# Performance work log

Hardware: AMD Instinct MI355X
Metric: run time of the kernel (lower is better)

Reference implementation:

```python
import jax, jax.numpy as jnp
import numpy as np

B, W, H, C = 4, 32, 32, 128   # image feature map
S, D = 256, 512               # text seq len, text embed dim
NC = 64                       # num_channels (attention inner dim)


def setup_inputs() -> dict:
    key = jax.random.key(0)
    ks = jax.random.split(key, 16)
    def dense(k, din, dout):
        return jax.random.normal(k, (din, dout), jnp.float32) / np.sqrt(din)
    return {
        "x": jax.random.normal(ks[0], (B, W, H, C), jnp.float32),
        "s": jax.random.normal(ks[1], (B, S, D), jnp.float32),
        "a": jax.random.randint(ks[2], (B, S), 0, 2).astype(jnp.float32),
        "Wq": dense(ks[3], C, NC),  "bq": jnp.zeros((NC,), jnp.float32),
        "Wkx": dense(ks[4], C, NC), "bkx": jnp.zeros((NC,), jnp.float32),
        "Wvx": dense(ks[5], C, NC), "bvx": jnp.zeros((NC,), jnp.float32),
        "Wks": dense(ks[6], D, NC), "bks": jnp.zeros((NC,), jnp.float32),
        "Wvs": dense(ks[7], D, NC), "bvs": jnp.zeros((NC,), jnp.float32),
        "Wout": dense(ks[8], NC, C), "bout": jnp.zeros((C,), jnp.float32),
        "ln_scale": jnp.ones((C,), jnp.float32),
        "ln_bias": jnp.zeros((C,), jnp.float32),
    }


def reference(x, s, a, Wq, bq, Wkx, bkx, Wvx, bvx, Wks, bks, Wvs, bvs,
              Wout, bout, ln_scale, ln_bias):
    nc = Wq.shape[-1]
    # mask text embeddings: repeat(a,'b s -> b s d') * s
    te = s * a[:, :, None]
    # projections
    q = x @ Wq + bq            # (b,w,h,c)
    kx = x @ Wkx + bkx         # (b,w,h,c)
    vx = x @ Vx_dummy if False else x @ Wvx + bvx
    ks = te @ Wks + bks        # (b,s,c)
    vs = te @ Wvs + bvs        # (b,s,c)
    # broadcast-add spatial and text keys/values -> (b,w,h,s,c)
    k = kx[:, :, :, None, :] + ks[:, None, None, :, :]
    v = vx[:, :, :, None, :] + vs[:, None, None, :, :]
    # attention matrix over channels: v^T @ k contracted over s -> (b,w,h,c,c)
    attn = jnp.einsum('bwhsc,bwhsd->bwhcd', v, k) / jnp.sqrt(jnp.asarray(nc, x.dtype))
    attn = jax.nn.softmax(attn, axis=-1)
    # q applied through the channel-channel attention -> (b,w,h,c)
    out = jnp.einsum('bwhj,bwhjk->bwhk', q, attn)
    # output projection back to x channels, residual, layernorm
    out = out @ Wout + bout
    x = x + out
    mu = jnp.mean(x, axis=-1, keepdims=True)
    var = jnp.var(x, axis=-1, keepdims=True)
    x = (x - mu) * jax.lax.rsqrt(var + 1e-6) * ln_scale + ln_bias
    return x
```

## Files before the change

kernel.cpp:

```cpp
#include <hip/hip_runtime.h>
#include <hip/hip_bf16.h>

#define BB 4
#define SS 256
#define DD 512
#define CC 128
#define NC 64
#define PXB 4

__global__ __launch_bounds__(256) void fused_proj_kernel(
    const float* __restrict__ x,
    const float* __restrict__ Wq,  const float* __restrict__ bq,
    const float* __restrict__ Wkx, const float* __restrict__ bkx,
    const float* __restrict__ Wvx, const float* __restrict__ bvx,
    const float* __restrict__ s, const float* __restrict__ a,
    const float* __restrict__ Wks, const float* __restrict__ bks,
    const float* __restrict__ Wvs, const float* __restrict__ bvs,
    float* __restrict__ P, float* __restrict__ ksw, float* __restrict__ vsw)
{
    __shared__ float tel[2][DD];
    __shared__ float part[2][2][2][NC];
    __shared__ float xl[8][CC];

    const int t = threadIdx.x;
    const int w = t >> 6, lane = t & 63;

    if (blockIdx.x < 512) {
        const int px0 = blockIdx.x * 8;
        {
            const float4* x4 = (const float4*)(x + (size_t)px0 * CC);
            ((float4*)&xl[0][0])[t] = x4[t];
        }
        __syncthreads();
        if (w < 3) {
            const float* __restrict__ Wm = (w == 0) ? Wq : (w == 1 ? Wkx : Wvx);
            const float* __restrict__ bm = (w == 0) ? bq : (w == 1 ? bkx : bvx);
            const int ksub = lane >> 4;
            const int cg = (lane & 15) * 4;
            float4 acc[8] = {};
            #pragma unroll 4
            for (int j = 0; j < 32; ++j) {
                const int k = 4 * j + ksub;
                const float4 wv = *(const float4*)(Wm + (size_t)k * NC + cg);
                #pragma unroll
                for (int px = 0; px < 8; ++px) {
                    const float xv = xl[px][k];
                    acc[px].x = fmaf(xv, wv.x, acc[px].x);
                    acc[px].y = fmaf(xv, wv.y, acc[px].y);
                    acc[px].z = fmaf(xv, wv.z, acc[px].z);
                    acc[px].w = fmaf(xv, wv.w, acc[px].w);
                }
            }
            #pragma unroll
            for (int px = 0; px < 8; ++px) {
                #pragma unroll
                for (int off = 16; off <= 32; off <<= 1) {
                    acc[px].x += __shfl_down(acc[px].x, off);
                    acc[px].y += __shfl_down(acc[px].y, off);
                    acc[px].z += __shfl_down(acc[px].z, off);
                    acc[px].w += __shfl_down(acc[px].w, off);
                }
            }
            if (ksub == 0) {
                const float4 bb = *(const float4*)(bm + cg);
                #pragma unroll
                for (int px = 0; px < 8; ++px) {
                    float4 v;
                    v.x = acc[px].x + bb.x; v.y = acc[px].y + bb.y;
                    v.z = acc[px].z + bb.z; v.w = acc[px].w + bb.w;
                    *(float4*)(P + (size_t)(px0 + px) * 192 + w * 64 + cg) = v;
                }
            }
        }
    } else {
        const int row0 = (blockIdx.x - 512) * 2;
        {
            const float4* s4 = (const float4*)(s + (size_t)row0 * DD);
            const int r = t >> 7;
            const float am = a[row0 + r];
            float4 v = s4[t];
            v.x *= am; v.y *= am; v.z *= am; v.w *= am;
            ((float4*)&tel[0][0])[t] = v;
        }
        __syncthreads();

        const int m = w & 1, h = w >> 1;
        const int kb = h * 256;
        const int cg = (lane & 15) * 4;
        const int ksub = lane >> 4;
        const float* __restrict__ Wm = m ? Wvs : Wks;

        float4 acc0 = {0,0,0,0}, acc1 = {0,0,0,0};
        #pragma unroll 4
        for (int j = 0; j < 64; ++j) {
            const int k = kb + 4 * j + ksub;
            const float4 wv = *(const float4*)(Wm + (size_t)k * NC + cg);
            const float t0 = tel[0][k];
            const float t1 = tel[1][k];
            acc0.x = fmaf(t0, wv.x, acc0.x); acc0.y = fmaf(t0, wv.y, acc0.y);
            acc0.z = fmaf(t0, wv.z, acc0.z); acc0.w = fmaf(t0, wv.w, acc0.w);
            acc1.x = fmaf(t1, wv.x, acc1.x); acc1.y = fmaf(t1, wv.y, acc1.y);
            acc1.z = fmaf(t1, wv.z, acc1.z); acc1.w = fmaf(t1, wv.w, acc1.w);
        }
        #pragma unroll
        for (int off = 16; off <= 32; off <<= 1) {
            acc0.x += __shfl_down(acc0.x, off); acc0.y += __shfl_down(acc0.y, off);
            acc0.z += __shfl_down(acc0.z, off); acc0.w += __shfl_down(acc0.w, off);
            acc1.x += __shfl_down(acc1.x, off); acc1.y += __shfl_down(acc1.y, off);
            acc1.z += __shfl_down(acc1.z, off); acc1.w += __shfl_down(acc1.w, off);
        }
        if (lane < 16) {
            *(float4*)&part[m][h][0][cg] = acc0;
            *(float4*)&part[m][h][1][cg] = acc1;
        }
        __syncthreads();

        {
            const int mm = t >> 7, r = (t >> 6) & 1, col = t & 63;
            const float v = part[mm][0][r][col] + part[mm][1][r][col]
                          + (mm ? bvs[col] : bks[col]);
            float* dst = mm ? vsw : ksw;
            dst[(size_t)(row0 + r) * NC + col] = v;
        }
    }
}

__global__ __launch_bounds__(256) void reduce_kernel(
    const float* __restrict__ ksw, const float* __restrict__ vsw,
    float* __restrict__ Mw, float* __restrict__ Ksw, float* __restrict__ Vsw)
{
    __shared__ float pm[4][NC], pk[4][NC], pv[4];
    const int t = threadIdx.x, w = t >> 6, d = t & 63;
    const int b = blockIdx.x >> 6, c = blockIdx.x & 63;
    const float* __restrict__ vsb = vsw + (size_t)b * SS * NC;
    const float* __restrict__ ksb = ksw + (size_t)b * SS * NC;
    float acc = 0.f, ks_ = 0.f, vs_ = 0.f;
    #pragma unroll 4
    for (int j = 0; j < 64; ++j) {
        const int s2 = w * 64 + j;
        const float vv = vsb[s2 * NC + c];
        const float kv = ksb[s2 * NC + d];
        acc = fmaf(vv, kv, acc);
        ks_ += kv; vs_ += vv;
    }
    pm[w][d] = acc; pk[w][d] = ks_;
    if (d == 0) pv[w] = vs_;
    __syncthreads();
    if (t < 64) {
        Mw[((size_t)b * NC + c) * NC + t] = pm[0][t] + pm[1][t] + pm[2][t] + pm[3][t];
        if (c == 0) Ksw[b * NC + t] = pk[0][t] + pk[1][t] + pk[2][t] + pk[3][t];
        if (t == 0) Vsw[b * NC + c] = pv[0] + pv[1] + pv[2] + pv[3];
    }
}

__global__ __launch_bounds__(256) void pixel_kernel(
    const float* __restrict__ x, const float* __restrict__ P,
    const float* __restrict__ Wout, const float* __restrict__ bout,
    const float* __restrict__ ln_scale, const float* __restrict__ ln_bias,
    const float* __restrict__ Mw, const float* __restrict__ Ksw,
    const float* __restrict__ Vsw,
    float* __restrict__ out)
{
    __shared__ float Ml[NC * 65];
    __shared__ float projl[PXB][192];
    __shared__ float xl[PXB][CC];
    __shared__ float rsl[PXB][NC];
    __shared__ float mxl[PXB][NC];
    __shared__ float outl[PXB][NC];
    __shared__ float Ksl[NC], Vsl[NC];
    __shared__ float redl[2][2][4];

    const int t = threadIdx.x;
    const int w = t >> 6, lane = t & 63;
    const int px0g = blockIdx.x * PXB;
    const int b = px0g >> 10;

    {
        const float4* P4 = (const float4*)(P + (size_t)px0g * 192);
        for (int i = t; i < PXB * 192 / 4; i += 256)
            ((float4*)&projl[0][0])[i] = P4[i];
        const float4* x4 = (const float4*)(x + (size_t)px0g * CC);
        for (int i = t; i < PXB * CC / 4; i += 256)
            ((float4*)&xl[0][0])[i] = x4[i];
        const float* Mb = Mw + (size_t)b * NC * NC;
        for (int i = t; i < NC * NC; i += 256)
            Ml[(i >> 6) * 65 + (i & 63)] = Mb[i];
        if (t < NC) { Ksl[t] = Ksw[b * NC + t]; Vsl[t] = Vsw[b * NC + t]; }
    }
    __syncthreads();

    {
        const int px = w, c = lane;
        const float vxc = projl[px][128 + c];
        const float qc  = projl[px][c];
        const float uc  = fmaf(256.0f, vxc, Vsl[c]);
        float mx = -3.4e38f;
        #pragma unroll
        for (int d = 0; d < NC; ++d) {
            const float A = fmaf(uc, projl[px][64 + d],
                                 fmaf(vxc, Ksl[d], Ml[c * 65 + d])) * 0.125f;
            mx = fmaxf(mx, A);
        }
        float sum = 0.f;
        #pragma unroll
        for (int d = 0; d < NC; ++d) {
            const float A = fmaf(uc, projl[px][64 + d],
                                 fmaf(vxc, Ksl[d], Ml[c * 65 + d])) * 0.125f;
            sum += __expf(A - mx);
        }
        rsl[px][c] = qc / sum;
        mxl[px][c] = mx;
    }
    __syncthreads();

    {
        const int px = w, d = lane;
        const float kxd = projl[px][64 + d];
        const float Ksd = Ksl[d];
        float acc = 0.f;
        #pragma unroll 4
        for (int c = 0; c < NC; ++c) {
            const float vxc = projl[px][128 + c];
            const float uc = fmaf(256.0f, vxc, Vsl[c]);
            const float A = fmaf(uc, kxd, fmaf(vxc, Ksd, Ml[c * 65 + d])) * 0.125f;
            acc = fmaf(rsl[px][c], __expf(A - mxl[px][c]), acc);
        }
        outl[px][d] = acc;
    }
    __syncthreads();

    {
        const int col = t & 127;
        const int pxg = t >> 7;
        const int px0 = 2 * pxg, px1 = px0 + 1;
        float acc0 = 0.f, acc1 = 0.f;
        #pragma unroll 4
        for (int k = 0; k < NC; ++k) {
            const float wv = Wout[k * CC + col];
            acc0 = fmaf(outl[px0][k], wv, acc0);
            acc1 = fmaf(outl[px1][k], wv, acc1);
        }
        const float bb = bout[col];
        const float y0 = acc0 + bb + xl[px0][col];
        const float y1 = acc1 + bb + xl[px1][col];

        float s10 = y0, s20 = y0 * y0, s11 = y1, s21 = y1 * y1;
        #pragma unroll
        for (int off = 32; off >= 1; off >>= 1) {
            s10 += __shfl_down(s10, off);
            s20 += __shfl_down(s20, off);
            s11 += __shfl_down(s11, off);
            s21 += __shfl_down(s21, off);
        }
        const int half = (t >> 6) & 1;
        if (lane == 0) {
            redl[pxg][half][0] = s10; redl[pxg][half][1] = s20;
            redl[pxg][half][2] = s11; redl[pxg][half][3] = s21;
        }
        __syncthreads();
        const float S10 = redl[pxg][0][0] + redl[pxg][1][0];
        const float S20 = redl[pxg][0][1] + redl[pxg][1][1];
        const float S11 = redl[pxg][0][2] + redl[pxg][1][2];
        const float S21 = redl[pxg][0][3] + redl[pxg][1][3];
        const float mu0 = S10 * (1.f / 128.f);
        const float var0 = S20 * (1.f / 128.f) - mu0 * mu0;
        const float mu1 = S11 * (1.f / 128.f);
        const float var1 = S21 * (1.f / 128.f) - mu1 * mu1;
        const float r0 = rsqrtf(var0 + 1e-6f), r1 = rsqrtf(var1 + 1e-6f);
        const float gg = ln_scale[col], be = ln_bias[col];
        out[(size_t)(px0g + px0) * CC + col] = (y0 - mu0) * r0 * gg + be;
        out[(size_t)(px0g + px1) * CC + col] = (y1 - mu1) * r1 * gg + be;
    }
}

extern "C" void kernel_launch(void* const* d_in, const int* in_sizes, int n_in,
                              void* d_out, int out_size, void* d_ws, size_t ws_size,
                              hipStream_t stream) {
    const float* x        = (const float*)d_in[0];
    const float* s        = (const float*)d_in[1];
    const float* a        = (const float*)d_in[2];
    const float* Wq       = (const float*)d_in[3];
    const float* bq       = (const float*)d_in[4];
    const float* Wkx      = (const float*)d_in[5];
    const float* bkx      = (const float*)d_in[6];
    const float* Wvx      = (const float*)d_in[7];
    const float* bvx      = (const float*)d_in[8];
    const float* Wks      = (const float*)d_in[9];
    const float* bks      = (const float*)d_in[10];
    const float* Wvs      = (const float*)d_in[11];
    const float* bvs      = (const float*)d_in[12];
    const float* Wout     = (const float*)d_in[13];
    const float* bout     = (const float*)d_in[14];
    const float* ln_scale = (const float*)d_in[15];
    const float* ln_bias  = (const float*)d_in[16];

    float* ws  = (float*)d_ws;
    float* ksw = ws;
    float* vsw = ws + 65536;
    float* Mw  = ws + 131072;
    float* Ksw = ws + 147456;
    float* Vsw = ws + 147712;
    float* Pw  = ws + 147968;

    fused_proj_kernel<<<1024, 256, 0, stream>>>(
        x, Wq, bq, Wkx, bkx, Wvx, bvx, s, a, Wks, bks, Wvs, bvs, Pw, ksw, vsw);
    reduce_kernel<<<BB * NC, 256, 0, stream>>>(ksw, vsw, Mw, Ksw, Vsw);
    pixel_kernel<<<(BB * 1024) / PXB, 256, 0, stream>>>(
        x, Pw, Wout, bout, ln_scale, ln_bias, Mw, Ksw, Vsw, (float*)d_out);
}
```

Before: 118.2 us.

## Fuse text-key/value reduction into projection kernel via atomics

Removes the separate reduce kernel. Each text block now projects 8 rows instead of 2 and computes its partial contributions to the channel-channel matrix M and to the key and value sums directly, accumulating them into global memory with atomicAdd after a memset. This saves a kernel launch and the workspace round trip for ks and vs. In exchange it adds 4096 atomics per text block across 128 blocks and a memset call, and the float summation order becomes nondeterministic.

```diff
diff --git a/kernel.cpp b/kernel.cpp
--- a/kernel.cpp
+++ b/kernel.cpp
@@ -7,44 +7,136 @@
 #define CC 128
 #define NC 64
 #define PXB 4
-
-__global__ __launch_bounds__(256) void fused_proj_kernel(
+#define NTEXT 128
+
+struct XRole { float xl[8][CC]; };
+struct TRole { float tel[8][DD];
+               float part[2][2][8][NC];
+               float ksl[8][NC]; float vsl[8][NC]; };
+union ProjSH { XRole xr; TRole tr; };
+
+__global__ __launch_bounds__(256) void proj_kernel(
     const float* __restrict__ x,
     const float* __restrict__ Wq,  const float* __restrict__ bq,
     const float* __restrict__ Wkx, const float* __restrict__ bkx,
     const float* __restrict__ Wvx, const float* __restrict__ bvx,
-    const float* __restrict__ s, const float* __restrict__ a,
+    const float* __restrict__ s,   const float* __restrict__ a,
     const float* __restrict__ Wks, const float* __restrict__ bks,
     const float* __restrict__ Wvs, const float* __restrict__ bvs,
-    float* __restrict__ P, float* __restrict__ ksw, float* __restrict__ vsw)
+    float* __restrict__ P, float* __restrict__ Mw,
+    float* __restrict__ Ksw, float* __restrict__ Vsw)
 {
-    __shared__ float tel[2][DD];
-    __shared__ float part[2][2][2][NC];
-    __shared__ float xl[8][CC];
-
+    __shared__ ProjSH sh;
     const int t = threadIdx.x;
     const int w = t >> 6, lane = t & 63;
-
-    if (blockIdx.x < 512) {
-        const int px0 = blockIdx.x * 8;
+    const int blk = blockIdx.x;
+
+    if (blk < NTEXT) {
+        const int row0 = blk * 8;
+        const int b = row0 >> 8;
         {
-            const float4* x4 = (const float4*)(x + (size_t)px0 * CC);
-            ((float4*)&xl[0][0])[t] = x4[t];
-        }
+            const float4* s4 = (const float4*)(s + (size_t)row0 * DD);
+            #pragma unroll
+            for (int j = 0; j < 4; ++j) {
+                const int i = t + j * 256;
+                const int r = i >> 7;
+                const float am = a[row0 + r];
+                float4 v = s4[i];
+                v.x *= am; v.y *= am; v.z *= am; v.w *= am;
+                ((float4*)&sh.tr.tel[0][0])[i] = v;
+            }
+        }
+        __syncthreads();
+
+        const int m = w & 1, h = w >> 1;
+        const int kb = h * 256;
+        const int cg4 = (lane & 15) * 4;
+        const int ksub = lane >> 4;
+        const float* __restrict__ Wm = m ? Wvs : Wks;
+
+        float4 acc[8] = {};
+        #pragma unroll 2
+        for (int j = 0; j < 64; ++j) {
+            const int k = kb + 4 * j + ksub;
+            const float4 wv = *(const float4*)(Wm + (size_t)k * NC + cg4);
+            #pragma unroll
+            for (int r = 0; r < 8; ++r) {
+                const float tv = sh.tr.tel[r][k];
+                acc[r].x = fmaf(tv, wv.x, acc[r].x);
+                acc[r].y = fmaf(tv, wv.y, acc[r].y);
+                acc[r].z = fmaf(tv, wv.z, acc[r].z);
+                acc[r].w = fmaf(tv, wv.w, acc[r].w);
+            }
+        }
+        #pragma unroll
+        for (int r = 0; r < 8; ++r) {
+            #pragma unroll
+            for (int off = 16; off <= 32; off <<= 1) {
+                acc[r].x += __shfl_down(acc[r].x, off);
+                acc[r].y += __shfl_down(acc[r].y, off);
+                acc[r].z += __shfl_down(acc[r].z, off);
+                acc[r].w += __shfl_down(acc[r].w, off);
+            }
+        }
+        if (lane < 16) {
+            #pragma unroll
+            for (int r = 0; r < 8; ++r)
+                *(float4*)&sh.tr.part[m][h][r][cg4] = acc[r];
+        }
+        __syncthreads();
+
+        #pragma unroll
+        for (int i = t; i < 1024; i += 256) {
+            const int mm = i >> 9;
+            const int r = (i >> 6) & 7;
+            const int col = i & 63;
+            const float v = sh.tr.part[mm][0][r][col] + sh.tr.part[mm][1][r][col]
+                          + (mm ? bvs[col] : bks[col]);
+            if (mm) sh.tr.vsl[r][col] = v; else sh.tr.ksl[r][col] = v;
+        }
+        __syncthreads();
+
+        if (w == 0) {
+            float sk = 0.f;
+            #pragma unroll
+            for (int r = 0; r < 8; ++r) sk += sh.tr.ksl[r][lane];
+            atomicAdd(&Ksw[b * NC + lane], sk);
+        } else if (w == 1) {
+            float sv = 0.f;
+            #pragma unroll
+            for (int r = 0; r < 8; ++r) sv += sh.tr.vsl[r][lane];
+            atomicAdd(&Vsw[b * NC + lane], sv);
+        }
+
+        float* __restrict__ Mb = Mw + (size_t)b * NC * NC;
+        #pragma unroll 4
+        for (int j = 0; j < 16; ++j) {
+            const int idx = t + j * 256;
+            const int c = idx >> 6;
+            float pm = 0.f;
+            #pragma unroll
+            for (int r = 0; r < 8; ++r)
+                pm = fmaf(sh.tr.vsl[r][c], sh.tr.ksl[r][lane], pm);
+            atomicAdd(Mb + idx, pm);
+        }
+    } else {
+        const int px0 = (blk - NTEXT) * 8;
+        ((float4*)&sh.xr.xl[0][0])[t] =
+            ((const float4*)(x + (size_t)px0 * CC))[t];
         __syncthreads();
         if (w < 3) {
             const float* __restrict__ Wm = (w == 0) ? Wq : (w == 1 ? Wkx : Wvx);
             const float* __restrict__ bm = (w == 0) ? bq : (w == 1 ? bkx : bvx);
             const int ksub = lane >> 4;
-            const int cg = (lane & 15) * 4;
+            const int cg4 = (lane & 15) * 4;
             float4 acc[8] = {};
             #pragma unroll 4
             for (int j = 0; j < 32; ++j) {
                 const int k = 4 * j + ksub;
-                const float4 wv = *(const float4*)(Wm + (size_t)k * NC + cg);
+                const float4 wv = *(const float4*)(Wm + (size_t)k * NC + cg4);
                 #pragma unroll
                 for (int px = 0; px < 8; ++px) {
-                    const float xv = xl[px][k];
+                    const float xv = sh.xr.xl[px][k];
                     acc[px].x = fmaf(xv, wv.x, acc[px].x);
                     acc[px].y = fmaf(xv, wv.y, acc[px].y);
                     acc[px].z = fmaf(xv, wv.z, acc[px].z);
@@ -62,94 +154,16 @@
                 }
             }
             if (ksub == 0) {
-                const float4 bb = *(const float4*)(bm + cg);
+                const float4 bb = *(const float4*)(bm + cg4);
                 #pragma unroll
                 for (int px = 0; px < 8; ++px) {
                     float4 v;
                     v.x = acc[px].x + bb.x; v.y = acc[px].y + bb.y;
                     v.z = acc[px].z + bb.z; v.w = acc[px].w + bb.w;
-                    *(float4*)(P + (size_t)(px0 + px) * 192 + w * 64 + cg) = v;
+                    *(float4*)(P + (size_t)(px0 + px) * 192 + w * 64 + cg4) = v;
                 }
             }
         }
-    } else {
-        const int row0 = (blockIdx.x - 512) * 2;
-        {
-            const float4* s4 = (const float4*)(s + (size_t)row0 * DD);
-            const int r = t >> 7;
-            const float am = a[row0 + r];
-            float4 v = s4[t];
-            v.x *= am; v.y *= am; v.z *= am; v.w *= am;
-            ((float4*)&tel[0][0])[t] = v;
-        }
-        __syncthreads();
-
-        const int m = w & 1, h = w >> 1;
-        const int kb = h * 256;
-        const int cg = (lane & 15) * 4;
-        const int ksub = lane >> 4;
-        const float* __restrict__ Wm = m ? Wvs : Wks;
-
-        float4 acc0 = {0,0,0,0}, acc1 = {0,0,0,0};
-        #pragma unroll 4
-        for (int j = 0; j < 64; ++j) {
-            const int k = kb + 4 * j + ksub;
-            const float4 wv = *(const float4*)(Wm + (size_t)k * NC + cg);
-            const float t0 = tel[0][k];
-            const float t1 = tel[1][k];
-            acc0.x = fmaf(t0, wv.x, acc0.x); acc0.y = fmaf(t0, wv.y, acc0.y);
-            acc0.z = fmaf(t0, wv.z, acc0.z); acc0.w = fmaf(t0, wv.w, acc0.w);
-            acc1.x = fmaf(t1, wv.x, acc1.x); acc1.y = fmaf(t1, wv.y, acc1.y);
-            acc1.z = fmaf(t1, wv.z, acc1.z); acc1.w = fmaf(t1, wv.w, acc1.w);
-        }
-        #pragma unroll
-        for (int off = 16; off <= 32; off <<= 1) {
-            acc0.x += __shfl_down(acc0.x, off); acc0.y += __shfl_down(acc0.y, off);
-            acc0.z += __shfl_down(acc0.z, off); acc0.w += __shfl_down(acc0.w, off);
-            acc1.x += __shfl_down(acc1.x, off); acc1.y += __shfl_down(acc1.y, off);
-            acc1.z += __shfl_down(acc1.z, off); acc1.w += __shfl_down(acc1.w, off);
-        }
-        if (lane < 16) {
-            *(float4*)&part[m][h][0][cg] = acc0;
-            *(float4*)&part[m][h][1][cg] = acc1;
-        }
-        __syncthreads();
-
-        {
-            const int mm = t >> 7, r = (t >> 6) & 1, col = t & 63;
-            const float v = part[mm][0][r][col] + part[mm][1][r][col]
-                          + (mm ? bvs[col] : bks[col]);
-            float* dst = mm ? vsw : ksw;
-            dst[(size_t)(row0 + r) * NC + col] = v;
-        }
-    }
-}
-
-__global__ __launch_bounds__(256) void reduce_kernel(
-    const float* __restrict__ ksw, const float* __restrict__ vsw,
-    float* __restrict__ Mw, float* __restrict__ Ksw, float* __restrict__ Vsw)
-{
-    __shared__ float pm[4][NC], pk[4][NC], pv[4];
-    const int t = threadIdx.x, w = t >> 6, d = t & 63;
-    const int b = blockIdx.x >> 6, c = blockIdx.x & 63;
-    const float* __restrict__ vsb = vsw + (size_t)b * SS * NC;
-    const float* __restrict__ ksb = ksw + (size_t)b * SS * NC;
-    float acc = 0.f, ks_ = 0.f, vs_ = 0.f;
-    #pragma unroll 4
-    for (int j = 0; j < 64; ++j) {
-        const int s2 = w * 64 + j;
-        const float vv = vsb[s2 * NC + c];
-        const float kv = ksb[s2 * NC + d];
-        acc = fmaf(vv, kv, acc);
-        ks_ += kv; vs_ += vv;
-    }
-    pm[w][d] = acc; pk[w][d] = ks_;
-    if (d == 0) pv[w] = vs_;
-    __syncthreads();
-    if (t < 64) {
-        Mw[((size_t)b * NC + c) * NC + t] = pm[0][t] + pm[1][t] + pm[2][t] + pm[3][t];
-        if (c == 0) Ksw[b * NC + t] = pk[0][t] + pk[1][t] + pk[2][t] + pk[3][t];
-        if (t == 0) Vsw[b * NC + c] = pv[0] + pv[1] + pv[2] + pv[3];
     }
 }
 
@@ -295,16 +309,16 @@
     const float* ln_bias  = (const float*)d_in[16];
 
     float* ws  = (float*)d_ws;
-    float* ksw = ws;
-    float* vsw = ws + 65536;
-    float* Mw  = ws + 131072;
-    float* Ksw = ws + 147456;
-    float* Vsw = ws + 147712;
-    float* Pw  = ws + 147968;
-
-    fused_proj_kernel<<<1024, 256, 0, stream>>>(
-        x, Wq, bq, Wkx, bkx, Wvx, bvx, s, a, Wks, bks, Wvs, bvs, Pw, ksw, vsw);
-    reduce_kernel<<<BB * NC, 256, 0, stream>>>(ksw, vsw, Mw, Ksw, Vsw);
+    float* Mw  = ws;
+    float* Ksw = ws + 16384;
+    float* Vsw = ws + 16640;
+    float* Pw  = ws + 16896;
+
+    hipMemsetAsync(Mw, 0, 16896 * sizeof(float), stream);
+
+    proj_kernel<<<NTEXT + 512, 256, 0, stream>>>(
+        x, Wq, bq, Wkx, bkx, Wvx, bvx, s, a, Wks, bks, Wvs, bvs,
+        Pw, Mw, Ksw, Vsw);
     pixel_kernel<<<(BB * 1024) / PXB, 256, 0, stream>>>(
         x, Pw, Wout, bout, ln_scale, ln_bias, Mw, Ksw, Vsw, (float*)d_out);
 }
```

Result: no change. 119.4 us (+1.0%).
